# Performance work log

Hardware: AMD Instinct MI355X
Metric: run time of the kernel (lower is better)

The kernel has to match this reference:

```python
import jax, jax.numpy as jnp
import numpy as np

N, E, C, NEF, OUT, NUM_ANGLE = 20000, 160000, 32, 1, 128, 7
F = 2 * C + NEF  # edge_fdim = 65


def setup_inputs() -> dict:
    rng = np.random.default_rng(0)
    row = rng.integers(0, N, size=E).astype(np.int32)
    col = rng.integers(0, N, size=E).astype(np.int32)
    # Line-graph incidence pairs (a, b): edge a = (i,j) feeds edge b = (j,k), i.e. col[a] == row[b].
    sort_idx = np.argsort(row, kind='stable')
    row_sorted = row[sort_idx]
    starts = np.searchsorted(row_sorted, col, 'left')
    ends = np.searchsorted(row_sorted, col, 'right')
    counts = ends - starts
    total = int(counts.sum())
    line_src = np.repeat(np.arange(E, dtype=np.int32), counts)
    base = np.repeat(starts, counts)
    within = np.arange(total, dtype=np.int64) - np.repeat(np.cumsum(counts) - counts, counts)
    line_dst = sort_idx[base + within].astype(np.int32)

    key = jax.random.key(0)
    k = jax.random.split(key, 5)
    return {
        'x': jax.random.normal(k[0], (N, C), jnp.float32),
        'edge_attr': jax.random.normal(k[1], (E, NEF), jnp.float32),
        'pos': jax.random.normal(k[2], (N, 3), jnp.float32),
        'W_msg': jax.random.normal(k[3], (OUT, NUM_ANGLE * 2 * F), jnp.float32) * 0.02,
        'b_msg': jax.random.normal(k[4], (OUT,), jnp.float32) * 0.01,
        'edge_index': jnp.asarray(np.stack([row, col]), jnp.int32),
        'line_src': jnp.asarray(line_src),
        'line_dst': jnp.asarray(line_dst),
    }


def reference(x, edge_attr, pos, W_msg, b_msg, edge_index, line_src, line_dst):
    row, col = edge_index[0], edge_index[1]
    num_node = x.shape[0]
    num_edge = row.shape[0]

    # edge_f = [x_row | x_col | edge_attr]  -> [E, F]
    edge_f = jnp.concatenate([x[row], x[col], edge_attr], axis=1)

    # Line graph: edge a=(i,j) feeds edge b=(j,k). Angle at shared node j.
    j = col[line_src]
    u = pos[row[line_src]] - pos[j]  # j -> i
    v = pos[col[line_dst]] - pos[j]  # j -> k
    cos = jnp.sum(u * v, axis=-1) / (
        jnp.linalg.norm(u, axis=-1) * jnp.linalg.norm(v, axis=-1) + 1e-8)
    ang = jnp.arccos(jnp.clip(cos, -1.0 + 1e-7, 1.0 - 1e-7))  # [0, pi]
    abin = jnp.clip((ang / jnp.pi * NUM_ANGLE).astype(jnp.int32), 0, NUM_ANGLE - 1)

    # Per target edge, accumulate neighbor-edge features into (angle bin, in/out slot).
    seg_in = line_dst.astype(jnp.int32) * (NUM_ANGLE * 2) + abin * 2      # incoming a -> b
    seg_out = line_src.astype(jnp.int32) * (NUM_ANGLE * 2) + abin * 2 + 1  # outgoing b seen from a
    vals = jnp.concatenate([edge_f[line_src], edge_f[line_dst]], axis=0)  # [2L, F]
    segs = jnp.concatenate([seg_in, seg_out], axis=0)
    msg = jax.ops.segment_sum(vals, segs, num_segments=num_edge * NUM_ANGLE * 2)
    msg = msg.reshape(num_edge, NUM_ANGLE * 2 * F)  # [E, 910]

    # output = self.message(message)  (Linear with bias)
    edge_hidden = msg @ W_msg.T + b_msg  # [E, OUT]

    # scatter_add into destination nodes (edge_index[1])
    update = jax.ops.segment_sum(edge_hidden, col, num_segments=num_node)  # [N, OUT]
    return update
```

## Files before the change

kernel.cpp:

```cpp
#include <hip/hip_runtime.h>
#include <stdint.h>

#define N_NODES 20000
#define E_EDGES 160000
#define C_DIM 32
#define OUT_DIM 128
#define K_REAL 910
#define KPH 480
#define DEG_CAP 64
#define SEG 1024
#define NSEG 20
#define MT_A (E_EDGES/256)
#define NROWS_B 20224
#define MT_B (NROWS_B/256)

typedef __attribute__((ext_vector_type(4))) float f32x4;
typedef __attribute__((ext_vector_type(8))) short short8;

__device__ __forceinline__ float bf2f(unsigned short u){
  union { unsigned int i; float f; } v; v.i = ((unsigned int)u) << 16; return v.f;
}
__device__ __forceinline__ unsigned short f2bf(float f){
  union { float f; unsigned int i; } v; v.f = f;
  unsigned int i = v.i;
  unsigned int r = (i + 0x7FFFu + ((i >> 16) & 1u)) >> 16;
  return (unsigned short)r;
}
__device__ __forceinline__ float ldv(const void* p, size_t i, int isbf){
  return isbf ? bf2f(((const unsigned short*)p)[i]) : ((const float*)p)[i];
}
__device__ __forceinline__ int clampi(int v, int hi){
  return ((unsigned)v < (unsigned)hi) ? v : 0;
}

__global__ void k_sniff(const void* xraw, int* flag){
  const unsigned short* xu = (const unsigned short*)xraw;
  __shared__ int s_bad;
  int tid = threadIdx.x;
  if (tid == 0) s_bad = 0;
  __syncthreads();
  float v = bf2f(xu[tid * 2499]);
  if (!(fabsf(v) < 100.0f)) s_bad = 1;
  __syncthreads();
  if (tid == 0) flag[0] = s_bad ? 0 : 1;
}

__global__ void k_zero(int* p, int n){
  int i = blockIdx.x*blockDim.x + threadIdx.x;
  if (i < n) p[i] = 0;
}

__global__ void k_build(const void* __restrict__ pos,
                        const int* __restrict__ row, const int* __restrict__ col,
                        float* __restrict__ vecn, int* __restrict__ cnt,
                        const int* __restrict__ flg)
{
  int e = blockIdx.x*blockDim.x + threadIdx.x;
  if (e >= E_EDGES) return;
  int isbf = flg[0];
  int r = clampi(row[e], N_NODES), c = clampi(col[e], N_NODES);
  float vx = ldv(pos, (size_t)c*3+0, isbf) - ldv(pos, (size_t)r*3+0, isbf);
  float vy = ldv(pos, (size_t)c*3+1, isbf) - ldv(pos, (size_t)r*3+1, isbf);
  float vz = ldv(pos, (size_t)c*3+2, isbf) - ldv(pos, (size_t)r*3+2, isbf);
  float nn = sqrtf(vx*vx + vy*vy + vz*vz);
  f32x4 vv; vv[0]=vx; vv[1]=vy; vv[2]=vz; vv[3]=nn;
  *(f32x4*)(vecn + (size_t)e*4) = vv;
  atomicAdd(cnt + r, 1);
  atomicAdd(cnt + N_NODES + c, 1);
}

__global__ void k_scan1(const int* __restrict__ cnt, int* __restrict__ start2,
                        int* __restrict__ segsum){
  __shared__ int buf[SEG];
  int b = blockIdx.x, arr = b / NSEG, seg = b - arr*NSEG;
  const int* cntp = cnt + (size_t)arr*N_NODES;
  int* startp = start2 + (size_t)arr*(N_NODES+1);
  int tid = threadIdx.x;
  int i = seg*SEG + tid;
  int v = (i < N_NODES) ? cntp[i] : 0;
  buf[tid] = v;
  __syncthreads();
  for (int off = 1; off < SEG; off <<= 1){
    int t = (tid >= off) ? buf[tid-off] : 0;
    __syncthreads();
    buf[tid] += t;
    __syncthreads();
  }
  if (i < N_NODES) startp[i] = buf[tid] - v;
  if (tid == SEG-1) segsum[b] = buf[tid];
}
__global__ void k_scan2(int* segsum){
  int tid = threadIdx.x;
  if (tid < 2){
    int run = 0;
    for (int s = 0; s < NSEG; ++s){
      int v = segsum[tid*NSEG+s]; segsum[tid*NSEG+s] = run; run += v;
    }
  }
}
__global__ void k_scan3(int* __restrict__ start2, int* __restrict__ fill2,
                        const int* __restrict__ segsum){
  int b = blockIdx.x, arr = b / NSEG, seg = b - arr*NSEG;
  int* startp = start2 + (size_t)arr*(N_NODES+1);
  int* fillp  = fill2  + (size_t)arr*N_NODES;
  int tid = threadIdx.x;
  int i = seg*SEG + tid;
  int add = segsum[b];
  if (i < N_NODES){ int s = startp[i] + add; startp[i] = s; fillp[i] = s; }
  if (b == 0 && tid == 0){
    start2[N_NODES] = E_EDGES;
    start2[(N_NODES+1) + N_NODES] = E_EDGES;
  }
}

__global__ void k_scatter(const int* __restrict__ row, const int* __restrict__ col,
                          int* fill2, int* list_row, int* list_col,
                          int* pos_col, int* node_of_pos)
{
  int e = blockIdx.x*blockDim.x + threadIdx.x;
  if (e >= E_EDGES) return;
  int r = clampi(row[e], N_NODES), c = clampi(col[e], N_NODES);
  int p = atomicAdd(fill2 + r, 1);
  if ((unsigned)p < E_EDGES) list_row[p] = e;
  int q = atomicAdd(fill2 + N_NODES + c, 1);
  if ((unsigned)q < E_EDGES){ list_col[q] = e; node_of_pos[q] = c; }
  pos_col[e] = clampi(q, E_EDGES);
}

__global__ void k_packw(const void* __restrict__ W, unsigned short* __restrict__ Wp,
                        const int* __restrict__ flg){
  int isbf = flg[0];
  int i = blockIdx.x*blockDim.x + threadIdx.x;
  if (i >= 2*OUT_DIM*KPH) return;
  int half = i / (OUT_DIM*KPH);
  int rem = i - half*OUT_DIM*KPH;
  int o = rem / KPH, kp = rem - o*KPH;
  float v = 0.f;
  if (kp < 455){
    int t = kp/65, f = kp - t*65;
    v = ldv(W, (size_t)o*K_REAL + (2*t + half)*65 + f, isbf);
  }
  Wp[i] = f2bf(v);
}

__global__ __launch_bounds__(256)
void k_msg_node(const void* __restrict__ x, const void* __restrict__ eattr,
                const float* __restrict__ vecn,
                const int* __restrict__ row, const int* __restrict__ col,
                const int* __restrict__ start2,
                const int* __restrict__ list_row, const int* __restrict__ list_col,
                const int* __restrict__ pos_col,
                unsigned short* __restrict__ msg,
                const int* __restrict__ flg, int half)
{
  __shared__ int posT[DEG_CAP];
  __shared__ int othS[DEG_CAP];
  __shared__ float vS[DEG_CAP][4], vT[DEG_CAP][4];
  __shared__ float eS[DEG_CAP];
  __shared__ unsigned short fS[DEG_CAP][64];
  __shared__ float e64[DEG_CAP][8];
  __shared__ unsigned char bins[DEG_CAP][DEG_CAP];

  const float cb1 = 0.9009688679f, cb2 = 0.6234898019f, cb3 = 0.2225209340f;
  const int* start_row = start2;
  const int* start_col = start2 + (N_NODES+1);
  int j = blockIdx.x;
  int tid = threadIdx.x, wv = tid >> 6, lane = tid & 63;
  int clo = start_col[j], chi = start_col[j+1];
  int rlo = start_row[j], rhi = start_row[j+1];
  if (clo < 0) clo = 0; if (chi > E_EDGES) chi = E_EDGES; if (chi < clo) chi = clo;
  if (rlo < 0) rlo = 0; if (rhi > E_EDGES) rhi = E_EDGES; if (rhi < rlo) rhi = rlo;
  int nI = chi - clo, nO = rhi - rlo;
  int nS = half ? nO : nI;
  int nT = half ? nI : nO;
  int slo = half ? rlo : clo;
  int tlo = half ? clo : rlo;
  const int* slist = half ? list_row : list_col;
  const int* tlist = half ? list_col : list_row;
  if (nT == 0) return;
  int isbf = flg[0];

  if (nS <= DEG_CAP && nT <= DEG_CAP){
    int nS4 = (nS + 3) & ~3;
    if (tid < nS){
      int s = clampi(slist[slo+tid], E_EDGES);
      othS[tid] = clampi(half ? col[s] : row[s], N_NODES);
      eS[tid] = ldv(eattr, s, isbf);
      vS[tid][0]=vecn[s*4+0]; vS[tid][1]=vecn[s*4+1];
      vS[tid][2]=vecn[s*4+2]; vS[tid][3]=vecn[s*4+3];
    }
    if (tid < nT){
      int t = clampi(tlist[tlo+tid], E_EDGES);
      posT[tid] = clampi(pos_col[t], E_EDGES);
      vT[tid][0]=vecn[t*4+0]; vT[tid][1]=vecn[t*4+1];
      vT[tid][2]=vecn[t*4+2]; vT[tid][3]=vecn[t*4+3];
    }
    for (int i = tid; i < DEG_CAP*8; i += 256) ((float*)e64)[i] = 0.f;
    { uint4 z = {0,0,0,0};
      ((uint4*)bins)[tid] = z; }
    __syncthreads();
    for (int cidx = tid; cidx < nS*64; cidx += 256){
      int si = cidx >> 6, f = cidx & 63;
      int lo_node = half ? j : othS[si];
      int hi_node = half ? othS[si] : j;
      int src = (f < 32) ? (lo_node*C_DIM + f) : (hi_node*C_DIM + f - 32);
      fS[si][f] = f2bf(ldv(x, (size_t)src, isbf));
    }
    for (int i = tid; i < (nS4 - nS)*64; i += 256)
      fS[nS + (i >> 6)][i & 63] = 0;
    for (int p = tid; p < nS*64; p += 256){
      int si = p >> 6, ti = p & 63;
      if (ti < nT){
        float dot = -(vS[si][0]*vT[ti][0] + vS[si][1]*vT[ti][1] + vS[si][2]*vT[ti][2]);
        float cv = dot / (vS[si][3]*vT[ti][3] + 1e-8f);
        int t = (cv<=cb1)+(cv<=cb2)+(cv<=cb3)+(cv<=-cb3)+(cv<=-cb2)+(cv<=-cb1);
        bins[ti][si] = (unsigned char)t;
        atomicAdd(&e64[ti][t], eS[si]);
      }
    }
    __syncthreads();
    for (int ti = wv; ti < nT; ti += 4){
      float S0=0,S1=0,S2=0,S3=0,S4=0,S5=0,S6=0;
      const unsigned* brow = (const unsigned*)bins[ti];
      for (int s4 = 0; s4 < nS4; s4 += 4){
        unsigned bb = (unsigned)__builtin_amdgcn_readfirstlane((int)brow[s4 >> 2]);
        #pragma unroll
        for (int u = 0; u < 4; ++u){
          int t = (bb >> (8*u)) & 7;
          float val = bf2f(fS[s4 + u][lane]);
          switch(t){
            case 0: S0+=val; break; case 1: S1+=val; break; case 2: S2+=val; break;
            case 3: S3+=val; break; case 4: S4+=val; break; case 5: S5+=val; break;
            default: S6+=val; break;
          }
        }
      }
      unsigned short* mrow = msg + (size_t)posT[ti]*KPH;
      mrow[0*65+lane]=f2bf(S0); mrow[1*65+lane]=f2bf(S1); mrow[2*65+lane]=f2bf(S2);
      mrow[3*65+lane]=f2bf(S3); mrow[4*65+lane]=f2bf(S4); mrow[5*65+lane]=f2bf(S5);
      mrow[6*65+lane]=f2bf(S6);
      if (lane < 7)  mrow[lane*65+64] = f2bf(e64[ti][lane]);
      if (lane < 25) mrow[455+lane] = 0;
    }
  } else {
    for (int ti = wv; ti < nT; ti += 4){
      int te = clampi(tlist[tlo+ti], E_EDGES);
      float tx=vecn[te*4+0], ty=vecn[te*4+1], tz=vecn[te*4+2], tn=vecn[te*4+3];
      float S0=0,S1=0,S2=0,S3=0,S4=0,S5=0,S6=0,S64v=0;
      for (int si = 0; si < nS; ++si){
        int se = clampi(slist[slo+si], E_EDGES);
        float dot = -(vecn[se*4+0]*tx + vecn[se*4+1]*ty + vecn[se*4+2]*tz);
        float cv = dot / (vecn[se*4+3]*tn + 1e-8f);
        int tv = (cv<=cb1)+(cv<=cb2)+(cv<=cb3)+(cv<=-cb3)+(cv<=-cb2)+(cv<=-cb1);
        int t = __builtin_amdgcn_readfirstlane(tv);
        int oth = clampi(half ? col[se] : row[se], N_NODES);
        int lo_node = half ? j : oth;
        int hi_node = half ? oth : j;
        float val = (lane < 32) ? ldv(x, (size_t)lo_node*C_DIM+lane, isbf)
                                : ldv(x, (size_t)hi_node*C_DIM+lane-32, isbf);
        switch(t){
          case 0: S0+=val; break; case 1: S1+=val; break; case 2: S2+=val; break;
          case 3: S3+=val; break; case 4: S4+=val; break; case 5: S5+=val; break;
          default: S6+=val; break;
        }
        S64v += (lane == t) ? ldv(eattr, se, isbf) : 0.f;
      }
      unsigned short* mrow = msg + (size_t)clampi(pos_col[te], E_EDGES)*KPH;
      mrow[0*65+lane]=f2bf(S0); mrow[1*65+lane]=f2bf(S1); mrow[2*65+lane]=f2bf(S2);
      mrow[3*65+lane]=f2bf(S3); mrow[4*65+lane]=f2bf(S4); mrow[5*65+lane]=f2bf(S5);
      mrow[6*65+lane]=f2bf(S6);
      if (lane < 7)  mrow[lane*65+64] = f2bf(S64v);
      if (lane < 25) mrow[455+lane] = 0;
    }
  }
}

__global__ __launch_bounds__(256)
void k_msg1(const void* __restrict__ x, const void* __restrict__ eattr,
            const float* __restrict__ vecn,
            const int* __restrict__ row, const int* __restrict__ col,
            const int* __restrict__ start2,
            const int* __restrict__ list_row, const int* __restrict__ list_col,
            unsigned short* __restrict__ msgN,
            const int* __restrict__ flg)
{
  const float cb1 = 0.9009688679f, cb2 = 0.6234898019f, cb3 = 0.2225209340f;
  const int* start_row = start2;
  const int* start_col = start2 + (N_NODES+1);
  int wv = threadIdx.x >> 6, lane = threadIdx.x & 63;
  int j = blockIdx.x*4 + wv;
  if (j >= N_NODES) return;
  int isbf = flg[0];
  unsigned short* mrow = msgN + (size_t)j*KPH;

  int clo = start_col[j], chi = start_col[j+1];
  int rlo = start_row[j], rhi = start_row[j+1];
  if (clo < 0) clo = 0; if (chi > E_EDGES) chi = E_EDGES; if (chi < clo) chi = clo;
  if (rlo < 0) rlo = 0; if (rhi > E_EDGES) rhi = E_EDGES; if (rhi < rlo) rhi = rlo;
  int nS = chi - clo, nT = rhi - rlo;

  if (nT == 0 || nS == 0){
    for (int i = lane; i < KPH; i += 64) mrow[i] = 0;
    return;
  }

  float xjv = ldv(x, (size_t)j*C_DIM + (lane & 31), isbf);

  int svalid = lane < nS;
  int se = svalid ? clampi(list_col[clo + lane], E_EDGES) : 0;
  f32x4 vs = *(const f32x4*)(vecn + (size_t)se*4);
  int multi = (nS > 64);

  float m0=0,m1=0,m2=0,m3=0,m4=0,m5=0,m6=0;
  float me0=0,me1=0,me2=0,me3=0,me4=0,me5=0,me6=0;

  for (int ti = 0; ti < nT; ++ti){
    int te = __builtin_amdgcn_readfirstlane(clampi(list_row[rlo+ti], E_EDGES));
    f32x4 vt = *(const f32x4*)(vecn + (size_t)te*4);
    int oT = clampi(col[te], N_NODES);
    float eTv = ldv(eattr, te, isbf);
    int c0=0,c1=0,c2=0,c3=0,c4=0,c5=0,c6=0;
    if (!multi){
      float dot = -(vs[0]*vt[0] + vs[1]*vt[1] + vs[2]*vt[2]);
      float cv = dot / (vs[3]*vt[3] + 1e-8f);
      int t = (cv<=cb1)+(cv<=cb2)+(cv<=cb3)+(cv<=-cb3)+(cv<=-cb2)+(cv<=-cb1);
      if (!svalid) t = 7;
      c0 = __popcll(__ballot(t==0)); c1 = __popcll(__ballot(t==1));
      c2 = __popcll(__ballot(t==2)); c3 = __popcll(__ballot(t==3));
      c4 = __popcll(__ballot(t==4)); c5 = __popcll(__ballot(t==5));
      c6 = __popcll(__ballot(t==6));
    } else {
      for (int base = 0; base < nS; base += 64){
        int vvalid = (base + lane) < nS;
        int s2 = vvalid ? clampi(list_col[clo + base + lane], E_EDGES) : 0;
        f32x4 v2 = *(const f32x4*)(vecn + (size_t)s2*4);
        float dot = -(v2[0]*vt[0] + v2[1]*vt[1] + v2[2]*vt[2]);
        float cv = dot / (v2[3]*vt[3] + 1e-8f);
        int t = (cv<=cb1)+(cv<=cb2)+(cv<=cb3)+(cv<=-cb3)+(cv<=-cb2)+(cv<=-cb1);
        if (!vvalid) t = 7;
        c0 += __popcll(__ballot(t==0)); c1 += __popcll(__ballot(t==1));
        c2 += __popcll(__ballot(t==2)); c3 += __popcll(__ballot(t==3));
        c4 += __popcll(__ballot(t==4)); c5 += __popcll(__ballot(t==5));
        c6 += __popcll(__ballot(t==6));
      }
    }
    float valT = (lane < 32) ? xjv : ldv(x, (size_t)oT*C_DIM + lane - 32, isbf);
    m0 += (float)c0*valT; m1 += (float)c1*valT; m2 += (float)c2*valT;
    m3 += (float)c3*valT; m4 += (float)c4*valT; m5 += (float)c5*valT;
    m6 += (float)c6*valT;
    me0 += (float)c0*eTv; me1 += (float)c1*eTv; me2 += (float)c2*eTv;
    me3 += (float)c3*eTv; me4 += (float)c4*eTv; me5 += (float)c5*eTv;
    me6 += (float)c6*eTv;
  }

  mrow[0*65+lane]=f2bf(m0); mrow[1*65+lane]=f2bf(m1); mrow[2*65+lane]=f2bf(m2);
  mrow[3*65+lane]=f2bf(m3); mrow[4*65+lane]=f2bf(m4); mrow[5*65+lane]=f2bf(m5);
  mrow[6*65+lane]=f2bf(m6);
  if (lane < 7){
    float me = (lane==0)?me0:(lane==1)?me1:(lane==2)?me2:(lane==3)?me3
             : (lane==4)?me4:(lane==5)?me5:me6;
    mrow[lane*65+64] = f2bf(me);
  }
  if (lane < 25) mrow[455+lane] = 0;
}

__global__ __launch_bounds__(256)
void k_gemm(const unsigned short* __restrict__ A,
            const unsigned short* __restrict__ Wp,
            const void* __restrict__ bias,
            const int* __restrict__ flg,
            const int* __restrict__ node_of_pos,
            float* __restrict__ out_acc, int addbias, int ident, int mtiles)
{
  __shared__ union {
    unsigned short Bs[64*512];
    float seg[256][66];
  } sh;
  __shared__ int nids[256];

  int tid = threadIdx.x;
  int w = tid >> 6, lane = tid & 63;
  int lrow = lane & 15, q = lane >> 4;

  int lin = blockIdx.x;
  const int FULLG = (mtiles & ~7) * 2;
  int mt, ch;
  if (lin < FULLG){
    mt = (lin >> 4)*8 + (lin & 7);
    ch = (lin >> 3) & 1;
  } else {
    int r2 = lin - FULLG;
    mt = (mtiles & ~7) + (r2 >> 1);
    ch = r2 & 1;
  }
  int m0 = mt * 256;

  nids[tid] = ident ? ((m0 + tid < N_NODES) ? m0 + tid : N_NODES-1)
                    : clampi(node_of_pos[m0 + tid], N_NODES);

  const unsigned short* abase = A + (size_t)(m0 + w*64 + lrow)*KPH + q*8;
  short8 apf[3][4];
  #pragma unroll
  for (int d = 0; d < 3; ++d)
    #pragma unroll
    for (int rf = 0; rf < 4; ++rf)
      apf[d][rf] = *(const short8*)(abase + (size_t)rf*16*KPH + d*32);

  #pragma unroll
  for (int i = 0; i < 15; ++i){
    int idx = tid + i*256;
    int rr = idx / 60, cc = idx - rr*60;
    const uint4* gq = (const uint4*)(Wp + (size_t)(ch*64 + rr)*KPH + cc*8);
    *(uint4*)(sh.Bs + rr*512 + ((cc ^ (rr & 7))*8)) = *gq;
  }
  __syncthreads();

  f32x4 acc[4][4];
  #pragma unroll
  for (int rf = 0; rf < 4; ++rf)
    #pragma unroll
    for (int nf = 0; nf < 4; ++nf) acc[rf][nf] = (f32x4)0.f;

  #pragma unroll
  for (int k0i = 0; k0i < 15; ++k0i){
    int cur = k0i % 3;
    int c = k0i*4 + q;
    #pragma unroll
    for (int nf = 0; nf < 4; ++nf){
      int rb = nf*16 + lrow;
      short8 bfr = *(const short8*)(sh.Bs + rb*512 + ((c ^ (rb & 7))*8));
      #pragma unroll
      for (int rf = 0; rf < 4; ++rf)
        acc[rf][nf] = __builtin_amdgcn_mfma_f32_16x16x32_bf16(apf[cur][rf], bfr, acc[rf][nf], 0, 0, 0);
    }
    if (k0i + 3 < 15){
      #pragma unroll
      for (int rf = 0; rf < 4; ++rf)
        apf[cur][rf] = *(const short8*)(abase + (size_t)rf*16*KPH + (k0i+3)*32);
    }
  }

  int isbf = flg[0];
  float bvs[4];
  #pragma unroll
  for (int nf = 0; nf < 4; ++nf)
    bvs[nf] = addbias ? ldv(bias, ch*64 + nf*16 + lrow, isbf) : 0.f;

  __syncthreads();
  #pragma unroll
  for (int rf = 0; rf < 4; ++rf)
    #pragma unroll
    for (int r = 0; r < 4; ++r){
      int m = w*64 + rf*16 + q*4 + r;
      #pragma unroll
      for (int nf = 0; nf < 4; ++nf)
        sh.seg[m][nf*16 + lrow] = acc[rf][nf][r] + bvs[nf];
    }
  __syncthreads();
  {
    int o = tid & 63, g = tid >> 6;
    int base = g*64;
    float s = 0.f;
    int curn = nids[base];
    for (int r = 0; r < 64; ++r){
      int m = base + r;
      int nid = nids[m];
      if (nid != curn){
        atomicAdd(out_acc + (size_t)curn*OUT_DIM + ch*64 + o, s);
        s = 0.f; curn = nid;
      }
      s += sh.seg[m][o];
    }
    atomicAdd(out_acc + (size_t)curn*OUT_DIM + ch*64 + o, s);
  }
}

__global__ void k_out(const float* __restrict__ acc, void* __restrict__ outp,
                      const int* __restrict__ flg){
  int i = blockIdx.x*blockDim.x + threadIdx.x;
  if (i >= N_NODES*OUT_DIM) return;
  if (flg[0]) ((unsigned short*)outp)[i] = f2bf(acc[i]);
  else        ((float*)outp)[i] = acc[i];
}

extern "C" void kernel_launch(void* const* d_in, const int* in_sizes, int n_in,
                              void* d_out, int out_size, void* d_ws, size_t ws_size,
                              hipStream_t stream)
{
  const void* x     = d_in[0];
  const void* eattr = d_in[1];
  const void* pos   = d_in[2];
  const void* W     = d_in[3];
  const void* bmsg  = d_in[4];
  const int* eidx = (const int*)d_in[5];
  const int* row = eidx;
  const int* col = eidx + E_EDGES;

  char* ws = (char*)d_ws;
  size_t off = 0;
  auto alloc = [&](size_t b){ size_t o = off; off += (b + 255) & ~(size_t)255; return o; };

  int* dflag        = (int*)(ws + alloc(256));
  float* vecn       = (float*)(ws + alloc((size_t)E_EDGES*16));
  int* cnt          = (int*)(ws + alloc((size_t)2*N_NODES*4));
  int* start2       = (int*)(ws + alloc((size_t)2*(N_NODES+1)*4));
  int* fill2        = (int*)(ws + alloc((size_t)2*N_NODES*4));
  int* segsum       = (int*)(ws + alloc((size_t)2*NSEG*4));
  int* list_row     = (int*)(ws + alloc((size_t)E_EDGES*4));
  int* list_col     = (int*)(ws + alloc((size_t)E_EDGES*4));
  int* pos_col      = (int*)(ws + alloc((size_t)E_EDGES*4));
  int* node_of_pos  = (int*)(ws + alloc((size_t)E_EDGES*4));
  unsigned short* Wp = (unsigned short*)(ws + alloc((size_t)2*OUT_DIM*KPH*2));
  float* out_acc    = (float*)(ws + alloc((size_t)N_NODES*OUT_DIM*4));
  unsigned short* msgN = (unsigned short*)(ws + alloc((size_t)NROWS_B*KPH*2));
  unsigned short* msg  = (unsigned short*)(ws + alloc((size_t)E_EDGES*KPH*2));
  (void)off;

  unsigned short* Wp_in  = Wp;
  unsigned short* Wp_out = Wp + (size_t)OUT_DIM*KPH;

  k_sniff<<<1, 256, 0, stream>>>(x, dflag);
  k_zero<<<(2*N_NODES+255)/256, 256, 0, stream>>>(cnt, 2*N_NODES);
  k_zero<<<(N_NODES*OUT_DIM+255)/256, 256, 0, stream>>>((int*)out_acc, N_NODES*OUT_DIM);
  {
    int padw = (NROWS_B - N_NODES)*KPH/2;
    k_zero<<<(padw+255)/256, 256, 0, stream>>>((int*)(msgN + (size_t)N_NODES*KPH), padw);
  }
  k_build<<<(E_EDGES+255)/256, 256, 0, stream>>>(pos, row, col, vecn, cnt, dflag);
  k_scan1<<<2*NSEG, SEG, 0, stream>>>(cnt, start2, segsum);
  k_scan2<<<1, 64, 0, stream>>>(segsum);
  k_scan3<<<2*NSEG, SEG, 0, stream>>>(start2, fill2, segsum);
  k_scatter<<<(E_EDGES+255)/256, 256, 0, stream>>>(row, col, fill2,
                                                   list_row, list_col, pos_col, node_of_pos);
  k_packw<<<(2*OUT_DIM*KPH+255)/256, 256, 0, stream>>>(W, Wp, dflag);

  k_msg_node<<<N_NODES, 256, 0, stream>>>(x, eattr, vecn, row, col, start2,
                                          list_row, list_col, pos_col, msg, dflag, 0);
  k_msg1<<<(N_NODES+3)/4, 256, 0, stream>>>(x, eattr, vecn, row, col, start2,
                                            list_row, list_col, msgN, dflag);
  k_gemm<<<dim3(2*MT_A), 256, 0, stream>>>(msg, Wp_in, bmsg, dflag,
                                           node_of_pos, out_acc, 1, 0, MT_A);
  k_gemm<<<dim3(2*MT_B), 256, 0, stream>>>(msgN, Wp_out, bmsg, dflag,
                                           node_of_pos, out_acc, 0, 1, MT_B);

  k_out<<<(N_NODES*OUT_DIM+255)/256, 256, 0, stream>>>(out_acc, d_out, dflag);
}
```

Before: 334.4 us.

## Precompute per-edge angle-bin counts and merge setup kernels

Adds a k_cnt kernel that computes, once per target edge, the packed angle-bin histogram of incoming source edges. k_msg1 then reads these packed counts instead of recomputing the ballots for every (target, source) pair, and processes targets in unrolled batches of eight via shuffles. The sniff and zero kernels are merged into one grid-stride init kernel, and the weight pack is merged into the build kernel, which cuts the number of launches. The cost is an extra E×8-byte buffer and one more launch. The counts are capped at 255 per bin.

```diff
diff --git a/kernel.cpp b/kernel.cpp
--- a/kernel.cpp
+++ b/kernel.cpp
@@ -13,6 +13,7 @@
 #define MT_A (E_EDGES/256)
 #define NROWS_B 20224
 #define MT_B (NROWS_B/256)
+#define PADW ((NROWS_B - N_NODES)*KPH/2)
 
 typedef __attribute__((ext_vector_type(4))) float f32x4;
 typedef __attribute__((ext_vector_type(8))) short short8;
@@ -33,40 +34,63 @@
   return ((unsigned)v < (unsigned)hi) ? v : 0;
 }
 
-__global__ void k_sniff(const void* xraw, int* flag){
-  const unsigned short* xu = (const unsigned short*)xraw;
-  __shared__ int s_bad;
+__global__ void k_init(const void* __restrict__ xraw, int* __restrict__ flag,
+                       int* __restrict__ cnt, float* __restrict__ out_acc,
+                       unsigned short* __restrict__ msgN)
+{
   int tid = threadIdx.x;
-  if (tid == 0) s_bad = 0;
-  __syncthreads();
-  float v = bf2f(xu[tid * 2499]);
-  if (!(fabsf(v) < 100.0f)) s_bad = 1;
-  __syncthreads();
-  if (tid == 0) flag[0] = s_bad ? 0 : 1;
-}
-
-__global__ void k_zero(int* p, int n){
-  int i = blockIdx.x*blockDim.x + threadIdx.x;
-  if (i < n) p[i] = 0;
-}
-
-__global__ void k_build(const void* __restrict__ pos,
-                        const int* __restrict__ row, const int* __restrict__ col,
-                        float* __restrict__ vecn, int* __restrict__ cnt,
-                        const int* __restrict__ flg)
-{
-  int e = blockIdx.x*blockDim.x + threadIdx.x;
-  if (e >= E_EDGES) return;
+  if (blockIdx.x == 0){
+    __shared__ int s_bad;
+    if (tid == 0) s_bad = 0;
+    __syncthreads();
+    float v = bf2f(((const unsigned short*)xraw)[tid * 2499]);
+    if (!(fabsf(v) < 100.0f)) s_bad = 1;
+    __syncthreads();
+    if (tid == 0) flag[0] = s_bad ? 0 : 1;
+  }
+  const int Z1 = 2*N_NODES;
+  const int Z2 = Z1 + N_NODES*OUT_DIM;
+  const int Z3 = Z2 + PADW;
+  int* padp = (int*)(msgN + (size_t)N_NODES*KPH);
+  for (int i = blockIdx.x*blockDim.x + tid; i < Z3; i += gridDim.x*blockDim.x){
+    if (i < Z1) cnt[i] = 0;
+    else if (i < Z2) ((int*)out_acc)[i - Z1] = 0;
+    else padp[i - Z2] = 0;
+  }
+}
+
+__global__ void k_prep(const void* __restrict__ pos, const void* __restrict__ W,
+                       const int* __restrict__ row, const int* __restrict__ col,
+                       float* __restrict__ vecn, int* __restrict__ cnt,
+                       unsigned short* __restrict__ Wp,
+                       const int* __restrict__ flg)
+{
   int isbf = flg[0];
-  int r = clampi(row[e], N_NODES), c = clampi(col[e], N_NODES);
-  float vx = ldv(pos, (size_t)c*3+0, isbf) - ldv(pos, (size_t)r*3+0, isbf);
-  float vy = ldv(pos, (size_t)c*3+1, isbf) - ldv(pos, (size_t)r*3+1, isbf);
-  float vz = ldv(pos, (size_t)c*3+2, isbf) - ldv(pos, (size_t)r*3+2, isbf);
-  float nn = sqrtf(vx*vx + vy*vy + vz*vz);
-  f32x4 vv; vv[0]=vx; vv[1]=vy; vv[2]=vz; vv[3]=nn;
-  *(f32x4*)(vecn + (size_t)e*4) = vv;
-  atomicAdd(cnt + r, 1);
-  atomicAdd(cnt + N_NODES + c, 1);
+  if (blockIdx.x < MT_A){
+    int e = blockIdx.x*256 + threadIdx.x;
+    if (e >= E_EDGES) return;
+    int r = clampi(row[e], N_NODES), c = clampi(col[e], N_NODES);
+    float vx = ldv(pos, (size_t)c*3+0, isbf) - ldv(pos, (size_t)r*3+0, isbf);
+    float vy = ldv(pos, (size_t)c*3+1, isbf) - ldv(pos, (size_t)r*3+1, isbf);
+    float vz = ldv(pos, (size_t)c*3+2, isbf) - ldv(pos, (size_t)r*3+2, isbf);
+    float nn = sqrtf(vx*vx + vy*vy + vz*vz);
+    f32x4 vv; vv[0]=vx; vv[1]=vy; vv[2]=vz; vv[3]=nn;
+    *(f32x4*)(vecn + (size_t)e*4) = vv;
+    atomicAdd(cnt + r, 1);
+    atomicAdd(cnt + N_NODES + c, 1);
+  } else {
+    int i = (blockIdx.x - MT_A)*256 + threadIdx.x;
+    if (i >= 2*OUT_DIM*KPH) return;
+    int half = i / (OUT_DIM*KPH);
+    int rem = i - half*OUT_DIM*KPH;
+    int o = rem / KPH, kp = rem - o*KPH;
+    float v = 0.f;
+    if (kp < 455){
+      int t = kp/65, f = kp - t*65;
+      v = ldv(W, (size_t)o*K_REAL + (2*t + half)*65 + f, isbf);
+    }
+    Wp[i] = f2bf(v);
+  }
 }
 
 __global__ void k_scan1(const int* __restrict__ cnt, int* __restrict__ start2,
@@ -125,22 +149,6 @@
   int q = atomicAdd(fill2 + N_NODES + c, 1);
   if ((unsigned)q < E_EDGES){ list_col[q] = e; node_of_pos[q] = c; }
   pos_col[e] = clampi(q, E_EDGES);
-}
-
-__global__ void k_packw(const void* __restrict__ W, unsigned short* __restrict__ Wp,
-                        const int* __restrict__ flg){
-  int isbf = flg[0];
-  int i = blockIdx.x*blockDim.x + threadIdx.x;
-  if (i >= 2*OUT_DIM*KPH) return;
-  int half = i / (OUT_DIM*KPH);
-  int rem = i - half*OUT_DIM*KPH;
-  int o = rem / KPH, kp = rem - o*KPH;
-  float v = 0.f;
-  if (kp < 455){
-    int t = kp/65, f = kp - t*65;
-    v = ldv(W, (size_t)o*K_REAL + (2*t + half)*65 + f, isbf);
-  }
-  Wp[i] = f2bf(v);
 }
 
 __global__ __launch_bounds__(256)
@@ -276,81 +284,110 @@
 }
 
 __global__ __launch_bounds__(256)
+void k_cnt(const float* __restrict__ vecn, const int* __restrict__ row,
+           const int* __restrict__ start2, const int* __restrict__ list_col,
+           const int* __restrict__ pos_col, uint2* __restrict__ cntb)
+{
+  int wv = threadIdx.x >> 6, lane = threadIdx.x & 63;
+  int b = blockIdx.x*4 + wv;
+  if (b >= E_EDGES) return;
+  const int* start_col = start2 + (N_NODES+1);
+  int j = clampi(row[b], N_NODES);
+  int clo = start_col[j], chi = start_col[j+1];
+  if (clo < 0) clo = 0; if (chi > E_EDGES) chi = E_EDGES; if (chi < clo) chi = clo;
+  int nS = chi - clo;
+  const float cb1 = 0.9009688679f, cb2 = 0.6234898019f, cb3 = 0.2225209340f;
+  f32x4 vt = *(const f32x4*)(vecn + (size_t)b*4);
+  unsigned n0=0,n1=0,n2=0,n3=0,n4=0,n5=0,n6=0;
+  for (int base = 0; base < nS; base += 64){
+    int ok = (base + lane) < nS;
+    int a = ok ? clampi(list_col[clo + base + lane], E_EDGES) : 0;
+    f32x4 va = *(const f32x4*)(vecn + (size_t)a*4);
+    float dot = -(va[0]*vt[0] + va[1]*vt[1] + va[2]*vt[2]);
+    float cv = dot / (va[3]*vt[3] + 1e-8f);
+    int t = (cv<=cb1)+(cv<=cb2)+(cv<=cb3)+(cv<=-cb3)+(cv<=-cb2)+(cv<=-cb1);
+    if (!ok) t = 7;
+    n0 += (unsigned)__popcll(__ballot(t==0));
+    n1 += (unsigned)__popcll(__ballot(t==1));
+    n2 += (unsigned)__popcll(__ballot(t==2));
+    n3 += (unsigned)__popcll(__ballot(t==3));
+    n4 += (unsigned)__popcll(__ballot(t==4));
+    n5 += (unsigned)__popcll(__ballot(t==5));
+    n6 += (unsigned)__popcll(__ballot(t==6));
+  }
+  if (lane == 0){
+    uint2 cw;
+    cw.x = min(n0,255u) | (min(n1,255u)<<8) | (min(n2,255u)<<16) | (min(n3,255u)<<24);
+    cw.y = min(n4,255u) | (min(n5,255u)<<8) | (min(n6,255u)<<16);
+    cntb[clampi(pos_col[b], E_EDGES)] = cw;
+  }
+}
+
+__global__ __launch_bounds__(256)
 void k_msg1(const void* __restrict__ x, const void* __restrict__ eattr,
-            const float* __restrict__ vecn,
-            const int* __restrict__ row, const int* __restrict__ col,
+            const int* __restrict__ col,
             const int* __restrict__ start2,
-            const int* __restrict__ list_row, const int* __restrict__ list_col,
+            const int* __restrict__ list_row, const int* __restrict__ pos_col,
+            const uint2* __restrict__ cntb,
             unsigned short* __restrict__ msgN,
             const int* __restrict__ flg)
 {
-  const float cb1 = 0.9009688679f, cb2 = 0.6234898019f, cb3 = 0.2225209340f;
-  const int* start_row = start2;
-  const int* start_col = start2 + (N_NODES+1);
   int wv = threadIdx.x >> 6, lane = threadIdx.x & 63;
   int j = blockIdx.x*4 + wv;
   if (j >= N_NODES) return;
   int isbf = flg[0];
   unsigned short* mrow = msgN + (size_t)j*KPH;
-
-  int clo = start_col[j], chi = start_col[j+1];
-  int rlo = start_row[j], rhi = start_row[j+1];
-  if (clo < 0) clo = 0; if (chi > E_EDGES) chi = E_EDGES; if (chi < clo) chi = clo;
+  int rlo = start2[j], rhi = start2[j+1];
   if (rlo < 0) rlo = 0; if (rhi > E_EDGES) rhi = E_EDGES; if (rhi < rlo) rhi = rlo;
-  int nS = chi - clo, nT = rhi - rlo;
-
-  if (nT == 0 || nS == 0){
+  int nT = rhi - rlo;
+  if (nT == 0){
     for (int i = lane; i < KPH; i += 64) mrow[i] = 0;
     return;
   }
-
-  float xjv = ldv(x, (size_t)j*C_DIM + (lane & 31), isbf);
-
-  int svalid = lane < nS;
-  int se = svalid ? clampi(list_col[clo + lane], E_EDGES) : 0;
-  f32x4 vs = *(const f32x4*)(vecn + (size_t)se*4);
-  int multi = (nS > 64);
-
+  float xj = ldv(x, (size_t)j*C_DIM + (lane & 31), isbf);
   float m0=0,m1=0,m2=0,m3=0,m4=0,m5=0,m6=0;
   float me0=0,me1=0,me2=0,me3=0,me4=0,me5=0,me6=0;
 
-  for (int ti = 0; ti < nT; ++ti){
-    int te = __builtin_amdgcn_readfirstlane(clampi(list_row[rlo+ti], E_EDGES));
-    f32x4 vt = *(const f32x4*)(vecn + (size_t)te*4);
-    int oT = clampi(col[te], N_NODES);
-    float eTv = ldv(eattr, te, isbf);
-    int c0=0,c1=0,c2=0,c3=0,c4=0,c5=0,c6=0;
-    if (!multi){
-      float dot = -(vs[0]*vt[0] + vs[1]*vt[1] + vs[2]*vt[2]);
-      float cv = dot / (vs[3]*vt[3] + 1e-8f);
-      int t = (cv<=cb1)+(cv<=cb2)+(cv<=cb3)+(cv<=-cb3)+(cv<=-cb2)+(cv<=-cb1);
-      if (!svalid) t = 7;
-      c0 = __popcll(__ballot(t==0)); c1 = __popcll(__ballot(t==1));
-      c2 = __popcll(__ballot(t==2)); c3 = __popcll(__ballot(t==3));
-      c4 = __popcll(__ballot(t==4)); c5 = __popcll(__ballot(t==5));
-      c6 = __popcll(__ballot(t==6));
-    } else {
-      for (int base = 0; base < nS; base += 64){
-        int vvalid = (base + lane) < nS;
-        int s2 = vvalid ? clampi(list_col[clo + base + lane], E_EDGES) : 0;
-        f32x4 v2 = *(const f32x4*)(vecn + (size_t)s2*4);
-        float dot = -(v2[0]*vt[0] + v2[1]*vt[1] + v2[2]*vt[2]);
-        float cv = dot / (v2[3]*vt[3] + 1e-8f);
-        int t = (cv<=cb1)+(cv<=cb2)+(cv<=cb3)+(cv<=-cb3)+(cv<=-cb2)+(cv<=-cb1);
-        if (!vvalid) t = 7;
-        c0 += __popcll(__ballot(t==0)); c1 += __popcll(__ballot(t==1));
-        c2 += __popcll(__ballot(t==2)); c3 += __popcll(__ballot(t==3));
-        c4 += __popcll(__ballot(t==4)); c5 += __popcll(__ballot(t==5));
-        c6 += __popcll(__ballot(t==6));
+  for (int tb = 0; tb < nT; tb += 64){
+    int nn = nT - tb; if (nn > 64) nn = 64;
+    int ok = lane < nn;
+    int te = ok ? clampi(list_row[rlo + tb + lane], E_EDGES) : 0;
+    int pp = clampi(pos_col[te], E_EDGES);
+    uint2 cw = cntb[pp];
+    int oL = clampi(col[te], N_NODES);
+    float eL = ok ? ldv(eattr, te, isbf) : 0.f;
+    unsigned cxL = ok ? cw.x : 0u;
+    unsigned cyL = ok ? cw.y : 0u;
+
+    for (int u = 0; u < nn; u += 8){
+      float v[8], ea[8];
+      unsigned cxa[8], cya[8];
+      #pragma unroll
+      for (int q = 0; q < 8; ++q){
+        int ti = u + q;
+        int o = __shfl(oL, ti);
+        unsigned cx = (unsigned)__shfl((int)cxL, ti);
+        unsigned cy = (unsigned)__shfl((int)cyL, ti);
+        float eb = __shfl(eL, ti);
+        if (ti < nn){
+          v[q] = (lane < 32) ? xj : ldv(x, (size_t)o*C_DIM + lane - 32, isbf);
+          cxa[q] = cx; cya[q] = cy; ea[q] = eb;
+        } else {
+          v[q] = 0.f; cxa[q] = 0u; cya[q] = 0u; ea[q] = 0.f;
+        }
       }
-    }
-    float valT = (lane < 32) ? xjv : ldv(x, (size_t)oT*C_DIM + lane - 32, isbf);
-    m0 += (float)c0*valT; m1 += (float)c1*valT; m2 += (float)c2*valT;
-    m3 += (float)c3*valT; m4 += (float)c4*valT; m5 += (float)c5*valT;
-    m6 += (float)c6*valT;
-    me0 += (float)c0*eTv; me1 += (float)c1*eTv; me2 += (float)c2*eTv;
-    me3 += (float)c3*eTv; me4 += (float)c4*eTv; me5 += (float)c5*eTv;
-    me6 += (float)c6*eTv;
+      #pragma unroll
+      for (int q = 0; q < 8; ++q){
+        float n0=(float)(cxa[q]&255u),  n1=(float)((cxa[q]>>8)&255u),
+              n2=(float)((cxa[q]>>16)&255u), n3=(float)(cxa[q]>>24),
+              n4=(float)(cya[q]&255u),  n5=(float)((cya[q]>>8)&255u),
+              n6=(float)((cya[q]>>16)&255u);
+        m0+=n0*v[q]; m1+=n1*v[q]; m2+=n2*v[q]; m3+=n3*v[q];
+        m4+=n4*v[q]; m5+=n5*v[q]; m6+=n6*v[q];
+        me0+=n0*ea[q]; me1+=n1*ea[q]; me2+=n2*ea[q]; me3+=n3*ea[q];
+        me4+=n4*ea[q]; me5+=n5*ea[q]; me6+=n6*ea[q];
+      }
+    }
   }
 
   mrow[0*65+lane]=f2bf(m0); mrow[1*65+lane]=f2bf(m1); mrow[2*65+lane]=f2bf(m2);
@@ -512,6 +549,7 @@
   int* node_of_pos  = (int*)(ws + alloc((size_t)E_EDGES*4));
   unsigned short* Wp = (unsigned short*)(ws + alloc((size_t)2*OUT_DIM*KPH*2));
   float* out_acc    = (float*)(ws + alloc((size_t)N_NODES*OUT_DIM*4));
+  uint2* cntb       = (uint2*)(ws + alloc((size_t)E_EDGES*8));
   unsigned short* msgN = (unsigned short*)(ws + alloc((size_t)NROWS_B*KPH*2));
   unsigned short* msg  = (unsigned short*)(ws + alloc((size_t)E_EDGES*KPH*2));
   (void)off;
@@ -519,25 +557,19 @@
   unsigned short* Wp_in  = Wp;
   unsigned short* Wp_out = Wp + (size_t)OUT_DIM*KPH;
 
-  k_sniff<<<1, 256, 0, stream>>>(x, dflag);
-  k_zero<<<(2*N_NODES+255)/256, 256, 0, stream>>>(cnt, 2*N_NODES);
-  k_zero<<<(N_NODES*OUT_DIM+255)/256, 256, 0, stream>>>((int*)out_acc, N_NODES*OUT_DIM);
-  {
-    int padw = (NROWS_B - N_NODES)*KPH/2;
-    k_zero<<<(padw+255)/256, 256, 0, stream>>>((int*)(msgN + (size_t)N_NODES*KPH), padw);
-  }
-  k_build<<<(E_EDGES+255)/256, 256, 0, stream>>>(pos, row, col, vecn, cnt, dflag);
+  k_init<<<2048, 256, 0, stream>>>(x, dflag, cnt, out_acc, msgN);
+  k_prep<<<MT_A + 480, 256, 0, stream>>>(pos, W, row, col, vecn, cnt, Wp, dflag);
   k_scan1<<<2*NSEG, SEG, 0, stream>>>(cnt, start2, segsum);
   k_scan2<<<1, 64, 0, stream>>>(segsum);
   k_scan3<<<2*NSEG, SEG, 0, stream>>>(start2, fill2, segsum);
   k_scatter<<<(E_EDGES+255)/256, 256, 0, stream>>>(row, col, fill2,
                                                    list_row, list_col, pos_col, node_of_pos);
-  k_packw<<<(2*OUT_DIM*KPH+255)/256, 256, 0, stream>>>(W, Wp, dflag);
 
   k_msg_node<<<N_NODES, 256, 0, stream>>>(x, eattr, vecn, row, col, start2,
                                           list_row, list_col, pos_col, msg, dflag, 0);
-  k_msg1<<<(N_NODES+3)/4, 256, 0, stream>>>(x, eattr, vecn, row, col, start2,
-                                            list_row, list_col, msgN, dflag);
+  k_cnt<<<(E_EDGES+3)/4, 256, 0, stream>>>(vecn, row, start2, list_col, pos_col, cntb);
+  k_msg1<<<(N_NODES+3)/4, 256, 0, stream>>>(x, eattr, col, start2,
+                                            list_row, pos_col, cntb, msgN, dflag);
   k_gemm<<<dim3(2*MT_A), 256, 0, stream>>>(msg, Wp_in, bmsg, dflag,
                                            node_of_pos, out_acc, 1, 0, MT_A);
   k_gemm<<<dim3(2*MT_B), 256, 0, stream>>>(msgN, Wp_out, bmsg, dflag,
```

New measurement: 342.9 us. +2.5%, slower.

## Merge setup kernels, single-block histogram scan, fuse two GEMM launches

Applied to the files above, without the earlier changes.

Cuts the kernel-launch count. The flag sniff and the zeroing passes merge into one init kernel, the position-vector build and weight packing share one launch, and the two GEMM launches become a single grid that picks its operand set from the block index. The global-atomic degree count plus the three-pass scan is replaced by a kernel that builds each histogram in 80KB of shared memory and scans it, with one 1024-thread block per array. That histogram step now runs on only two blocks and serialises 160k shared atomics per block, so it may be slower than the old wide global-atomic pass.

```diff
diff --git a/kernel.cpp b/kernel.cpp
--- a/kernel.cpp
+++ b/kernel.cpp
@@ -8,11 +8,10 @@
 #define K_REAL 910
 #define KPH 480
 #define DEG_CAP 64
-#define SEG 1024
-#define NSEG 20
 #define MT_A (E_EDGES/256)
 #define NROWS_B 20224
 #define MT_B (NROWS_B/256)
+#define PADW ((NROWS_B - N_NODES)*KPH/2)
 
 typedef __attribute__((ext_vector_type(4))) float f32x4;
 typedef __attribute__((ext_vector_type(8))) short short8;
@@ -33,84 +32,106 @@
   return ((unsigned)v < (unsigned)hi) ? v : 0;
 }
 
-__global__ void k_sniff(const void* xraw, int* flag){
-  const unsigned short* xu = (const unsigned short*)xraw;
-  __shared__ int s_bad;
+__global__ void k_init(const void* __restrict__ xraw, int* __restrict__ flag,
+                       float* __restrict__ out_acc, unsigned short* __restrict__ msgN)
+{
   int tid = threadIdx.x;
-  if (tid == 0) s_bad = 0;
+  if (blockIdx.x == 0){
+    __shared__ int s_bad;
+    if (tid == 0) s_bad = 0;
+    __syncthreads();
+    float v = bf2f(((const unsigned short*)xraw)[tid * 2499]);
+    if (!(fabsf(v) < 100.0f)) s_bad = 1;
+    __syncthreads();
+    if (tid == 0) flag[0] = s_bad ? 0 : 1;
+  }
+  const int Z1 = N_NODES*OUT_DIM;
+  const int Z2 = Z1 + PADW;
+  int* padp = (int*)(msgN + (size_t)N_NODES*KPH);
+  for (int i = blockIdx.x*blockDim.x + tid; i < Z2; i += gridDim.x*blockDim.x){
+    if (i < Z1) ((int*)out_acc)[i] = 0;
+    else padp[i - Z1] = 0;
+  }
+}
+
+__global__ void k_prep(const void* __restrict__ pos, const void* __restrict__ W,
+                       const int* __restrict__ row, const int* __restrict__ col,
+                       float* __restrict__ vecn, unsigned short* __restrict__ Wp,
+                       const int* __restrict__ flg)
+{
+  int isbf = flg[0];
+  if (blockIdx.x < MT_A){
+    int e = blockIdx.x*256 + threadIdx.x;
+    if (e >= E_EDGES) return;
+    int r = clampi(row[e], N_NODES), c = clampi(col[e], N_NODES);
+    float vx = ldv(pos, (size_t)c*3+0, isbf) - ldv(pos, (size_t)r*3+0, isbf);
+    float vy = ldv(pos, (size_t)c*3+1, isbf) - ldv(pos, (size_t)r*3+1, isbf);
+    float vz = ldv(pos, (size_t)c*3+2, isbf) - ldv(pos, (size_t)r*3+2, isbf);
+    float nn = sqrtf(vx*vx + vy*vy + vz*vz);
+    f32x4 vv; vv[0]=vx; vv[1]=vy; vv[2]=vz; vv[3]=nn;
+    *(f32x4*)(vecn + (size_t)e*4) = vv;
+  } else {
+    int i = (blockIdx.x - MT_A)*256 + threadIdx.x;
+    if (i >= 2*OUT_DIM*KPH) return;
+    int half = i / (OUT_DIM*KPH);
+    int rem = i - half*OUT_DIM*KPH;
+    int o = rem / KPH, kp = rem - o*KPH;
+    float v = 0.f;
+    if (kp < 455){
+      int t = kp/65, f = kp - t*65;
+      v = ldv(W, (size_t)o*K_REAL + (2*t + half)*65 + f, isbf);
+    }
+    Wp[i] = f2bf(v);
+  }
+}
+
+__global__ __launch_bounds__(1024)
+void k_histscan(const int* __restrict__ row, const int* __restrict__ col,
+                int* __restrict__ start2, int* __restrict__ fill2)
+{
+  __shared__ int h[N_NODES];
+  __shared__ int wsum[16];
+  __shared__ int carry;
+  int arr = blockIdx.x;
+  const int* ids = arr ? col : row;
+  int tid = threadIdx.x, lane = tid & 63, w = tid >> 6;
+  for (int i = tid; i < N_NODES; i += 1024) h[i] = 0;
+  if (tid == 0) carry = 0;
   __syncthreads();
-  float v = bf2f(xu[tid * 2499]);
-  if (!(fabsf(v) < 100.0f)) s_bad = 1;
+  for (int e = tid; e < E_EDGES; e += 1024)
+    atomicAdd(&h[clampi(ids[e], N_NODES)], 1);
   __syncthreads();
-  if (tid == 0) flag[0] = s_bad ? 0 : 1;
-}
-
-__global__ void k_zero(int* p, int n){
-  int i = blockIdx.x*blockDim.x + threadIdx.x;
-  if (i < n) p[i] = 0;
-}
-
-__global__ void k_build(const void* __restrict__ pos,
-                        const int* __restrict__ row, const int* __restrict__ col,
-                        float* __restrict__ vecn, int* __restrict__ cnt,
-                        const int* __restrict__ flg)
-{
-  int e = blockIdx.x*blockDim.x + threadIdx.x;
-  if (e >= E_EDGES) return;
-  int isbf = flg[0];
-  int r = clampi(row[e], N_NODES), c = clampi(col[e], N_NODES);
-  float vx = ldv(pos, (size_t)c*3+0, isbf) - ldv(pos, (size_t)r*3+0, isbf);
-  float vy = ldv(pos, (size_t)c*3+1, isbf) - ldv(pos, (size_t)r*3+1, isbf);
-  float vz = ldv(pos, (size_t)c*3+2, isbf) - ldv(pos, (size_t)r*3+2, isbf);
-  float nn = sqrtf(vx*vx + vy*vy + vz*vz);
-  f32x4 vv; vv[0]=vx; vv[1]=vy; vv[2]=vz; vv[3]=nn;
-  *(f32x4*)(vecn + (size_t)e*4) = vv;
-  atomicAdd(cnt + r, 1);
-  atomicAdd(cnt + N_NODES + c, 1);
-}
-
-__global__ void k_scan1(const int* __restrict__ cnt, int* __restrict__ start2,
-                        int* __restrict__ segsum){
-  __shared__ int buf[SEG];
-  int b = blockIdx.x, arr = b / NSEG, seg = b - arr*NSEG;
-  const int* cntp = cnt + (size_t)arr*N_NODES;
-  int* startp = start2 + (size_t)arr*(N_NODES+1);
-  int tid = threadIdx.x;
-  int i = seg*SEG + tid;
-  int v = (i < N_NODES) ? cntp[i] : 0;
-  buf[tid] = v;
-  __syncthreads();
-  for (int off = 1; off < SEG; off <<= 1){
-    int t = (tid >= off) ? buf[tid-off] : 0;
-    __syncthreads();
-    buf[tid] += t;
-    __syncthreads();
-  }
-  if (i < N_NODES) startp[i] = buf[tid] - v;
-  if (tid == SEG-1) segsum[b] = buf[tid];
-}
-__global__ void k_scan2(int* segsum){
-  int tid = threadIdx.x;
-  if (tid < 2){
-    int run = 0;
-    for (int s = 0; s < NSEG; ++s){
-      int v = segsum[tid*NSEG+s]; segsum[tid*NSEG+s] = run; run += v;
-    }
-  }
-}
-__global__ void k_scan3(int* __restrict__ start2, int* __restrict__ fill2,
-                        const int* __restrict__ segsum){
-  int b = blockIdx.x, arr = b / NSEG, seg = b - arr*NSEG;
   int* startp = start2 + (size_t)arr*(N_NODES+1);
   int* fillp  = fill2  + (size_t)arr*N_NODES;
-  int tid = threadIdx.x;
-  int i = seg*SEG + tid;
-  int add = segsum[b];
-  if (i < N_NODES){ int s = startp[i] + add; startp[i] = s; fillp[i] = s; }
-  if (b == 0 && tid == 0){
-    start2[N_NODES] = E_EDGES;
-    start2[(N_NODES+1) + N_NODES] = E_EDGES;
-  }
+  for (int base = 0; base < N_NODES; base += 1024){
+    int i = base + tid;
+    int v = (i < N_NODES) ? h[i] : 0;
+    int s = v;
+    #pragma unroll
+    for (int off = 1; off < 64; off <<= 1){
+      int t = __shfl_up(s, off);
+      if (lane >= off) s += t;
+    }
+    if (lane == 63) wsum[w] = s;
+    __syncthreads();
+    if (w == 0){
+      int t = (lane < 16) ? wsum[lane] : 0;
+      #pragma unroll
+      for (int off = 1; off < 16; off <<= 1){
+        int u = __shfl_up(t, off);
+        if (lane >= off) t += u;
+      }
+      if (lane < 16) wsum[lane] = t;
+    }
+    __syncthreads();
+    int woff = (w > 0) ? wsum[w-1] : 0;
+    int exc = s + woff + carry - v;
+    if (i < N_NODES){ startp[i] = exc; fillp[i] = exc; }
+    __syncthreads();
+    if (tid == 0) carry += wsum[15];
+    __syncthreads();
+  }
+  if (tid == 0) startp[N_NODES] = E_EDGES;
 }
 
 __global__ void k_scatter(const int* __restrict__ row, const int* __restrict__ col,
@@ -125,22 +146,6 @@
   int q = atomicAdd(fill2 + N_NODES + c, 1);
   if ((unsigned)q < E_EDGES){ list_col[q] = e; node_of_pos[q] = c; }
   pos_col[e] = clampi(q, E_EDGES);
-}
-
-__global__ void k_packw(const void* __restrict__ W, unsigned short* __restrict__ Wp,
-                        const int* __restrict__ flg){
-  int isbf = flg[0];
-  int i = blockIdx.x*blockDim.x + threadIdx.x;
-  if (i >= 2*OUT_DIM*KPH) return;
-  int half = i / (OUT_DIM*KPH);
-  int rem = i - half*OUT_DIM*KPH;
-  int o = rem / KPH, kp = rem - o*KPH;
-  float v = 0.f;
-  if (kp < 455){
-    int t = kp/65, f = kp - t*65;
-    v = ldv(W, (size_t)o*K_REAL + (2*t + half)*65 + f, isbf);
-  }
-  Wp[i] = f2bf(v);
 }
 
 __global__ __launch_bounds__(256)
@@ -365,12 +370,14 @@
 }
 
 __global__ __launch_bounds__(256)
-void k_gemm(const unsigned short* __restrict__ A,
-            const unsigned short* __restrict__ Wp,
-            const void* __restrict__ bias,
-            const int* __restrict__ flg,
-            const int* __restrict__ node_of_pos,
-            float* __restrict__ out_acc, int addbias, int ident, int mtiles)
+void k_gemmN(const unsigned short* __restrict__ msg,
+             const unsigned short* __restrict__ Wp_in,
+             const unsigned short* __restrict__ msgN,
+             const unsigned short* __restrict__ Wp_out,
+             const void* __restrict__ bias,
+             const int* __restrict__ flg,
+             const int* __restrict__ node_of_pos,
+             float* __restrict__ out_acc)
 {
   __shared__ union {
     unsigned short Bs[64*512];
@@ -382,7 +389,14 @@
   int w = tid >> 6, lane = tid & 63;
   int lrow = lane & 15, q = lane >> 4;
 
-  int lin = blockIdx.x;
+  int which = (blockIdx.x >= 2*MT_A) ? 1 : 0;
+  int lin = blockIdx.x - which*2*MT_A;
+  const unsigned short* A  = which ? msgN  : msg;
+  const unsigned short* Wp = which ? Wp_out : Wp_in;
+  int mtiles  = which ? MT_B : MT_A;
+  int addbias = !which;
+  int ident   = which;
+
   const int FULLG = (mtiles & ~7) * 2;
   int mt, ch;
   if (lin < FULLG){
@@ -502,10 +516,8 @@
 
   int* dflag        = (int*)(ws + alloc(256));
   float* vecn       = (float*)(ws + alloc((size_t)E_EDGES*16));
-  int* cnt          = (int*)(ws + alloc((size_t)2*N_NODES*4));
   int* start2       = (int*)(ws + alloc((size_t)2*(N_NODES+1)*4));
   int* fill2        = (int*)(ws + alloc((size_t)2*N_NODES*4));
-  int* segsum       = (int*)(ws + alloc((size_t)2*NSEG*4));
   int* list_row     = (int*)(ws + alloc((size_t)E_EDGES*4));
   int* list_col     = (int*)(ws + alloc((size_t)E_EDGES*4));
   int* pos_col      = (int*)(ws + alloc((size_t)E_EDGES*4));
@@ -519,29 +531,16 @@
   unsigned short* Wp_in  = Wp;
   unsigned short* Wp_out = Wp + (size_t)OUT_DIM*KPH;
 
-  k_sniff<<<1, 256, 0, stream>>>(x, dflag);
-  k_zero<<<(2*N_NODES+255)/256, 256, 0, stream>>>(cnt, 2*N_NODES);
-  k_zero<<<(N_NODES*OUT_DIM+255)/256, 256, 0, stream>>>((int*)out_acc, N_NODES*OUT_DIM);
-  {
-    int padw = (NROWS_B - N_NODES)*KPH/2;
-    k_zero<<<(padw+255)/256, 256, 0, stream>>>((int*)(msgN + (size_t)N_NODES*KPH), padw);
-  }
-  k_build<<<(E_EDGES+255)/256, 256, 0, stream>>>(pos, row, col, vecn, cnt, dflag);
-  k_scan1<<<2*NSEG, SEG, 0, stream>>>(cnt, start2, segsum);
-  k_scan2<<<1, 64, 0, stream>>>(segsum);
-  k_scan3<<<2*NSEG, SEG, 0, stream>>>(start2, fill2, segsum);
+  k_init<<<2048, 256, 0, stream>>>(x, dflag, out_acc, msgN);
+  k_prep<<<MT_A + 480, 256, 0, stream>>>(pos, W, row, col, vecn, Wp, dflag);
+  k_histscan<<<2, 1024, 0, stream>>>(row, col, start2, fill2);
   k_scatter<<<(E_EDGES+255)/256, 256, 0, stream>>>(row, col, fill2,
                                                    list_row, list_col, pos_col, node_of_pos);
-  k_packw<<<(2*OUT_DIM*KPH+255)/256, 256, 0, stream>>>(W, Wp, dflag);
-
   k_msg_node<<<N_NODES, 256, 0, stream>>>(x, eattr, vecn, row, col, start2,
                                           list_row, list_col, pos_col, msg, dflag, 0);
   k_msg1<<<(N_NODES+3)/4, 256, 0, stream>>>(x, eattr, vecn, row, col, start2,
                                             list_row, list_col, msgN, dflag);
-  k_gemm<<<dim3(2*MT_A), 256, 0, stream>>>(msg, Wp_in, bmsg, dflag,
-                                           node_of_pos, out_acc, 1, 0, MT_A);
-  k_gemm<<<dim3(2*MT_B), 256, 0, stream>>>(msgN, Wp_out, bmsg, dflag,
-                                           node_of_pos, out_acc, 0, 1, MT_B);
-
+  k_gemmN<<<dim3(2*MT_A + 2*MT_B), 256, 0, stream>>>(msg, Wp_in, msgN, Wp_out,
+                                                     bmsg, dflag, node_of_pos, out_acc);
   k_out<<<(N_NODES*OUT_DIM+255)/256, 256, 0, stream>>>(out_acc, d_out, dflag);
 }
```

Result: slower. 360.6 us (+7.8%).
